# Kernel optimization log

Measured on AMD Instinct MI355X. Metric: run time of the kernel, lower is better.

The kernel has to match this reference:

```python
import jax, jax.numpy as jnp
import numpy as np

GAMMA = 0.3
R_PERCENT = 0.2
LAMBDA_PENALTY = 0.5
EPS = 1e-06

B_SZ, N_HEADS, K_FULL = 16, 32, 32768
K_IMG = 16384


def _zscore(x):
    mu = x.mean(axis=-1, keepdims=True)
    std = jnp.sqrt(((x - mu) ** 2).mean(axis=-1, keepdims=True))  # unbiased=False
    return (x - mu) / (std + EPS)


def _topk_binary(scores, k):
    # scores: [B,H] -> binary mask [B,H]; only strictly-positive topk values count
    vals, idx = jax.lax.top_k(scores, k)
    b = jnp.arange(scores.shape[0])[:, None]
    return jnp.zeros_like(scores).at[b, idx].set((vals > 0).astype(scores.dtype))


def setup_inputs() -> dict:
    key = jax.random.key(0)
    k1, k2, k3, k4, k5 = jax.random.split(key, 5)
    attn_logits_last = jax.random.normal(k1, (B_SZ, N_HEADS, K_FULL), dtype=jnp.float32)
    # exactly K_IMG image tokens per row (alternating pattern -> strided gather)
    image_mask = jnp.tile((jnp.arange(K_FULL) % 2 == 0).astype(jnp.int32)[None, :], (B_SZ, 1))
    feat_C = jax.random.normal(k2, (B_SZ, K_IMG), dtype=jnp.float32)
    feat_A = jax.random.normal(k3, (B_SZ, K_IMG), dtype=jnp.float32)
    feat_D = jax.random.normal(k4, (B_SZ, K_IMG), dtype=jnp.float32)
    feat_B = jax.random.normal(k5, (B_SZ, K_IMG), dtype=jnp.float32)
    return {"attn_logits_last": attn_logits_last, "image_mask": image_mask,
            "feat_C": feat_C, "feat_A": feat_A, "feat_D": feat_D, "feat_B": feat_B}


def reference(attn_logits_last, image_mask, feat_C, feat_A, feat_D, feat_B):
    B, H, K_full = attn_logits_last.shape
    K_img = feat_C.shape[1]

    # --- compute_rf ---
    C_t = jax.nn.relu(_zscore(feat_C))
    A_t = jax.nn.sigmoid(_zscore(feat_A))
    D_t = jax.nn.sigmoid(_zscore(feat_D))
    B_t = jax.nn.sigmoid(_zscore(feat_B))
    denom = jnp.maximum(1.0 + LAMBDA_PENALTY * (D_t + B_t), EPS)
    rf = jnp.maximum(C_t * A_t / denom, 0.0)  # [B,K_img]

    # --- align: positions of image tokens (exactly K_img ones per row) ---
    idx = jax.vmap(lambda m: jnp.nonzero(m, size=K_img)[0])(image_mask)  # [B,K_img]

    # --- image-normalized attention ---
    probs_full = jax.nn.softmax(attn_logits_last, axis=-1)
    mask_f = image_mask[:, None, :].astype(attn_logits_last.dtype)  # [B,1,K_full]
    probs_img = probs_full * mask_f
    probs_img_norm = probs_img / jnp.maximum(probs_img.sum(axis=-1, keepdims=True), EPS)
    attn_img_norm = jnp.take_along_axis(probs_img_norm, idx[:, None, :], axis=-1)  # [B,H,K_img]

    # --- dynamic head roles ---
    low_rf = jnp.maximum(1.0 - rf, 0.0)
    s_pos = (attn_img_norm * rf[:, None, :]).sum(axis=-1)   # [B,H]
    s_neg = (attn_img_norm * low_rf[:, None, :]).sum(axis=-1)
    k_heads = min(max(1, int(np.ceil(R_PERCENT * H))), H)
    m_pos = _topk_binary(s_pos, k_heads)
    neg_scores = jnp.where(m_pos > 0, -jnp.inf, s_neg)
    m_neg = _topk_binary(neg_scores, k_heads) * (m_pos == 0).astype(s_pos.dtype)

    # --- delta and scatter back to full logits ---
    delta_img = GAMMA * (m_pos[:, :, None] * rf[:, None, :]
                         - m_neg[:, :, None] * low_rf[:, None, :])  # [B,H,K_img]
    delta_full = jax.vmap(
        lambda d, i: jnp.zeros((H, K_full), attn_logits_last.dtype).at[:, i].set(d)
    )(delta_img, idx)
    delta_full = delta_full * mask_f
    return attn_logits_last + delta_full
```

## Files before the change

### kernel.cpp

```cpp
#include <hip/hip_runtime.h>
#include <math.h>

#define GAMMA 0.3f
#define EPS 1e-6f
#define B_SZ 16
#define NH 32
#define KF 32768
#define KI 16384
#define KHEADS 7

typedef float f4v __attribute__((ext_vector_type(4)));

constexpr int OFF_MU    = 0;
constexpr int OFF_SD    = 64;
constexpr int OFF_RAWS  = 128;
constexpr int OFF_RAWP  = 640;
constexpr int OFF_RAWN  = 1152;
constexpr int IOFF_BSUM = 1664;
constexpr int OFF_RFF   = 4096;


__global__ __launch_bounds__(256) void k_stats_cnt(const float* __restrict__ fC,
        const float* __restrict__ fA, const float* __restrict__ fD,
        const float* __restrict__ fB, const int* __restrict__ mask,
        float* __restrict__ ws) {
    int bid = blockIdx.x, t = threadIdx.x;
    int lane = t & 63, wid = t >> 6;
    if (bid < 64) {
        int b = bid >> 2, f = bid & 3;
        const float* src;
        if (f == 0) src = fC; else if (f == 1) src = fA; else if (f == 2) src = fD; else src = fB;
        src += (size_t)b * KI;
        double s = 0.0, s2 = 0.0;
        #pragma unroll 4
        for (int i = t; i < KI / 4; i += 256) {
            float4 v = ((const float4*)src)[i];
            s  += (double)v.x + (double)v.y + (double)v.z + (double)v.w;
            s2 += (double)v.x * v.x + (double)v.y * v.y + (double)v.z * v.z + (double)v.w * v.w;
        }
        #pragma unroll
        for (int off = 32; off > 0; off >>= 1) {
            s  += __shfl_down(s, off);
            s2 += __shfl_down(s2, off);
        }
        __shared__ double w1[4], w2[4];
        if (lane == 0) { w1[wid] = s; w2[wid] = s2; }
        __syncthreads();
        if (t == 0) {
            double S1 = w1[0] + w1[1] + w1[2] + w1[3];
            double S2 = w2[0] + w2[1] + w2[2] + w2[3];
            double mu  = S1 * (1.0 / KI);
            double var = fmax(S2 * (1.0 / KI) - mu * mu, 0.0);
            ws[OFF_MU + bid] = (float)mu;
            ws[OFF_SD + bid] = (float)(sqrt(var) + (double)EPS);
        }
    } else {
        int cblk = bid - 64;
        if (cblk < 6) ws[OFF_RAWS + cblk * 256 + t] = 0.f;
        const int* mrow = mask + (size_t)cblk * 2048;
        int4 m0 = *(const int4*)(mrow + t * 8);
        int4 m1 = *(const int4*)(mrow + t * 8 + 4);
        int cnt = (m0.x != 0) + (m0.y != 0) + (m0.z != 0) + (m0.w != 0)
                + (m1.x != 0) + (m1.y != 0) + (m1.z != 0) + (m1.w != 0);
        #pragma unroll
        for (int off = 32; off > 0; off >>= 1) cnt += __shfl_down(cnt, off);
        __shared__ int wc[4];
        if (lane == 0) wc[wid] = cnt;
        __syncthreads();
        if (t == 0) ((int*)ws)[IOFF_BSUM + cblk] = wc[0] + wc[1] + wc[2] + wc[3];
    }
}

__global__ __launch_bounds__(256) void k_rf_expand(const float* __restrict__ fC,
        const float* __restrict__ fA, const float* __restrict__ fD,
        const float* __restrict__ fB, const int* __restrict__ mask,
        float* __restrict__ ws) {
    __shared__ int sb[16];
    __shared__ int wsum[4];
    __shared__ float rfbuf[2048];
    int blk = blockIdx.x, t = threadIdx.x;
    int b = blk >> 4, c = blk & 15;
    int lane = t & 63, wid = t >> 6;

    const int* bsum = (const int*)ws + IOFF_BSUM;
    if (t < 16) sb[t] = (t < c) ? bsum[(b << 4) + t] : 0;

    const int* mrow = mask + (size_t)blk * 2048;
    int4 m0 = *(const int4*)(mrow + t * 8);
    int4 m1 = *(const int4*)(mrow + t * 8 + 4);
    int mv[8] = {m0.x, m0.y, m0.z, m0.w, m1.x, m1.y, m1.z, m1.w};
    int cnt = 0;
    #pragma unroll
    for (int j = 0; j < 8; ++j) cnt += (mv[j] != 0);

    int x = cnt;
    #pragma unroll
    for (int off = 1; off < 64; off <<= 1) {
        int v = __shfl_up(x, off);
        if (lane >= off) x += v;
    }
    if (lane == 63) wsum[wid] = x;
    __syncthreads();
    int base = 0;
    #pragma unroll
    for (int w = 0; w < 4; ++w) base += (w < wid) ? wsum[w] : 0;
    int total = wsum[0] + wsum[1] + wsum[2] + wsum[3];
    int rloc = base + x - cnt;
    int boff = 0;
    #pragma unroll
    for (int i = 0; i < 16; ++i) boff += sb[i];

    float mu0 = ws[OFF_MU + b * 4 + 0], sd0 = ws[OFF_SD + b * 4 + 0];
    float mu1 = ws[OFF_MU + b * 4 + 1], sd1 = ws[OFF_SD + b * 4 + 1];
    float mu2 = ws[OFF_MU + b * 4 + 2], sd2 = ws[OFF_SD + b * 4 + 2];
    float mu3 = ws[OFF_MU + b * 4 + 3], sd3 = ws[OFF_SD + b * 4 + 3];
    for (int j = t; j < total; j += 256) {
        size_t idx = (size_t)b * KI + boff + j;
        float Ct = fmaxf((fC[idx] - mu0) / sd0, 0.f);
        float At = 1.f / (1.f + __expf(-((fA[idx] - mu1) / sd1)));
        float Dt = 1.f / (1.f + __expf(-((fD[idx] - mu2) / sd2)));
        float Bt = 1.f / (1.f + __expf(-((fB[idx] - mu3) / sd3)));
        float denom = fmaxf(1.f + 0.5f * (Dt + Bt), EPS);
        rfbuf[j] = fmaxf(Ct * At / denom, 0.f);
    }
    __syncthreads();
    float vr[8];
    #pragma unroll
    for (int j = 0; j < 8; ++j) {
        if (mv[j]) { vr[j] = rfbuf[rloc]; ++rloc; }
        else       { vr[j] = -1.f; }
    }
    float* rff = ws + OFF_RFF + (size_t)blk * 2048 + t * 8;
    *(float4*)(rff)     = *(float4*)(vr);
    *(float4*)(rff + 4) = *(float4*)(vr + 4);
}

__global__ __launch_bounds__(256) void k_scores(const float* __restrict__ attn,
                                                float* __restrict__ ws) {
    int g = blockIdx.x, t = threadIdx.x;
    int bh = g >> 2, qtr = g & 3;
    int b = bh >> 5;
    const float* xr  = attn + ((size_t)bh << 15) + ((size_t)qtr << 13);
    const float* rff = ws + OFF_RFF + ((size_t)b << 15) + ((size_t)qtr << 13);
    float S = 0.f, P = 0.f, N = 0.f;
    #pragma unroll
    for (int i = 0; i < 8; ++i) {
        int k = (i * 256 + t) * 4;
        float4 xs = *(const float4*)(xr + k);
        float4 rv = *(const float4*)(rff + k);
        float xa[4] = {xs.x, xs.y, xs.z, xs.w};
        float va[4] = {rv.x, rv.y, rv.z, rv.w};
        #pragma unroll
        for (int j = 0; j < 4; ++j) {
            float e = __expf(xa[j]);
            bool on = va[j] >= 0.f;
            float rfv  = fmaxf(va[j], 0.f);
            float lrfv = on ? fmaxf(1.f - va[j], 0.f) : 0.f;
            S += on ? e : 0.f;
            P = fmaf(e, rfv, P);
            N = fmaf(e, lrfv, N);
        }
    }
    int lane = t & 63, wid = t >> 6;
    #pragma unroll
    for (int off = 32; off > 0; off >>= 1) {
        S += __shfl_down(S, off);
        P += __shfl_down(P, off);
        N += __shfl_down(N, off);
    }
    __shared__ float wS[4], wP[4], wN[4];
    if (lane == 0) { wS[wid] = S; wP[wid] = P; wN[wid] = N; }
    __syncthreads();
    if (t == 0) {
        atomicAdd(&ws[OFF_RAWS + bh], wS[0] + wS[1] + wS[2] + wS[3]);
        atomicAdd(&ws[OFF_RAWP + bh], wP[0] + wP[1] + wP[2] + wP[3]);
        atomicAdd(&ws[OFF_RAWN + bh], wN[0] + wN[1] + wN[2] + wN[3]);
    }
}

__global__ __launch_bounds__(256) void k_out(const float* __restrict__ attn,
        const float* __restrict__ ws, float* __restrict__ out) {
    unsigned int t = threadIdx.x;
    unsigned int j = blockIdx.x;
    unsigned int r = j & 7, q = j >> 3;
    unsigned int chunk = 8u * r + 64u * (q >> 3) + (q & 7);
    unsigned int flat = chunk * 2048 + t * 8;
    unsigned int bh = flat >> 15;
    unsigned int b  = bh >> 5;
    unsigned int h  = bh & 31;

    __shared__ float ssp[NH], snv[NH];
    __shared__ int smp[NH];
    __shared__ float s_gp, s_gn;
    if (t < NH) {
        float S0 = ws[OFF_RAWS + b * NH + t];
        ssp[t] = ws[OFF_RAWP + b * NH + t] / S0;
        snv[t] = ws[OFF_RAWN + b * NH + t] / S0;
    }
    __syncthreads();
    if (t < NH) {
        float sp = ssp[t];
        int cnt = 0;
        for (int jj = 0; jj < NH; ++jj) { float o = ssp[jj]; cnt += (o > sp) || (o == sp && jj < (int)t); }
        smp[t] = (cnt < KHEADS) && (sp > 0.f);
    }
    __syncthreads();
    if (t < NH && smp[t]) snv[t] = -INFINITY;
    __syncthreads();
    if (t == 0) {
        float gp = 0.f, gn = 0.f;
        if (smp[h]) gp = GAMMA;
        else {
            float nv = snv[h];
            int cnt = 0;
            for (int jj = 0; jj < NH; ++jj) { float o = snv[jj]; cnt += (o > nv) || (o == nv && jj < (int)h); }
            if ((cnt < KHEADS) && (nv > 0.f)) gn = GAMMA;
        }
        s_gp = gp; s_gn = gn;
    }
    __syncthreads();

    float gp = s_gp, gn = s_gn;
    const float* rff = ws + OFF_RFF + ((size_t)b << 15);
    unsigned int k = flat & (KF - 1);
    #pragma unroll
    for (int half8 = 0; half8 < 2; ++half8) {
        unsigned int f2 = flat + half8 * 4, k2 = k + half8 * 4;
        float4 xs = *(const float4*)(attn + f2);
        float4 rv = *(const float4*)(rff + k2);
        float va[4] = {rv.x, rv.y, rv.z, rv.w};
        float xa[4] = {xs.x, xs.y, xs.z, xs.w};
        float oa[4];
        #pragma unroll
        for (int jj = 0; jj < 4; ++jj) {
            bool on = va[jj] >= 0.f;
            float rfv  = fmaxf(va[jj], 0.f);
            float lrfv = on ? fmaxf(1.f - va[jj], 0.f) : 0.f;
            oa[jj] = xa[jj] + gp * rfv - gn * lrfv;
        }
        f4v o = {oa[0], oa[1], oa[2], oa[3]};
        __builtin_nontemporal_store(o, (f4v*)(out + f2));
    }
}

extern "C" void kernel_launch(void* const* d_in, const int* in_sizes, int n_in,
                              void* d_out, int out_size, void* d_ws, size_t ws_size,
                              hipStream_t stream) {
    const float* attn = (const float*)d_in[0];
    const int*   mask = (const int*)d_in[1];
    const float* fC   = (const float*)d_in[2];
    const float* fA   = (const float*)d_in[3];
    const float* fD   = (const float*)d_in[4];
    const float* fB   = (const float*)d_in[5];
    float* out = (float*)d_out;
    float* ws = (float*)d_ws;

    k_stats_cnt<<<320, 256, 0, stream>>>(fC, fA, fD, fB, mask, ws);
    k_rf_expand<<<256, 256, 0, stream>>>(fC, fA, fD, fB, mask, ws);
    k_scores   <<<2048, 256, 0, stream>>>(attn, ws);
    k_out      <<<B_SZ * NH * KF / 2048, 256, 0, stream>>>(attn, ws, out);
}
```

Measured before the change: 147.2 us.

## Compute head-role gains once in last-block epilogue of reduction kernel

Adds a per-batch completion counter to the score-reduction kernel so that the last block for each batch computes the top-k head masks and writes per-head gp/gn gains to the workspace. The output kernel then just loads two scalars per block, instead of every block redoing the ranking with several __syncthreads barriers. The attention input is also read with nontemporal loads. In exchange, the reduction kernel gains threadfences, a counter atomic and a serialized tail block.

```diff
diff --git a/kernel.cpp b/kernel.cpp
--- a/kernel.cpp
+++ b/kernel.cpp
@@ -16,7 +16,10 @@
 constexpr int OFF_RAWS  = 128;
 constexpr int OFF_RAWP  = 640;
 constexpr int OFF_RAWN  = 1152;
-constexpr int IOFF_BSUM = 1664;
+constexpr int OFF_GP    = 1664;
+constexpr int OFF_GN    = 2176;
+constexpr int IOFF_CNT  = 2688;
+constexpr int IOFF_BSUM = 2720;
 constexpr int OFF_RFF   = 4096;
 
 
@@ -57,6 +60,7 @@
     } else {
         int cblk = bid - 64;
         if (cblk < 6) ws[OFF_RAWS + cblk * 256 + t] = 0.f;
+        if (cblk == 6 && t < 16) ((int*)ws)[IOFF_CNT + t] = 0;
         const int* mrow = mask + (size_t)cblk * 2048;
         int4 m0 = *(const int4*)(mrow + t * 8);
         int4 m1 = *(const int4*)(mrow + t * 8 + 4);
@@ -169,12 +173,51 @@
         N += __shfl_down(N, off);
     }
     __shared__ float wS[4], wP[4], wN[4];
+    __shared__ int s_last;
     if (lane == 0) { wS[wid] = S; wP[wid] = P; wN[wid] = N; }
     __syncthreads();
     if (t == 0) {
         atomicAdd(&ws[OFF_RAWS + bh], wS[0] + wS[1] + wS[2] + wS[3]);
         atomicAdd(&ws[OFF_RAWP + bh], wP[0] + wP[1] + wP[2] + wP[3]);
         atomicAdd(&ws[OFF_RAWN + bh], wN[0] + wN[1] + wN[2] + wN[3]);
+        __threadfence();
+        int old = atomicAdd((int*)ws + IOFF_CNT + b, 1);
+        s_last = (old == 127);
+    }
+    __syncthreads();
+    if (!s_last) return;
+
+    __threadfence();
+    __shared__ float ssp[NH], snv[NH];
+    __shared__ int smp[NH];
+    if (t < NH) {
+        float S0 = __hip_atomic_load(&ws[OFF_RAWS + b * NH + t], __ATOMIC_RELAXED, __HIP_MEMORY_SCOPE_AGENT);
+        float Pp = __hip_atomic_load(&ws[OFF_RAWP + b * NH + t], __ATOMIC_RELAXED, __HIP_MEMORY_SCOPE_AGENT);
+        float Nn = __hip_atomic_load(&ws[OFF_RAWN + b * NH + t], __ATOMIC_RELAXED, __HIP_MEMORY_SCOPE_AGENT);
+        ssp[t] = Pp / S0;
+        snv[t] = Nn / S0;
+    }
+    __syncthreads();
+    if (t < NH) {
+        float sp = ssp[t];
+        int c2 = 0;
+        for (int j = 0; j < NH; ++j) { float o = ssp[j]; c2 += (o > sp) || (o == sp && j < t); }
+        smp[t] = (c2 < KHEADS) && (sp > 0.f);
+    }
+    __syncthreads();
+    if (t < NH && smp[t]) snv[t] = -INFINITY;
+    __syncthreads();
+    if (t < NH) {
+        float gp = 0.f, gn = 0.f;
+        if (smp[t]) gp = GAMMA;
+        else {
+            float nv = snv[t];
+            int c2 = 0;
+            for (int j = 0; j < NH; ++j) { float o = snv[j]; c2 += (o > nv) || (o == nv && j < t); }
+            if ((c2 < KHEADS) && (nv > 0.f)) gn = GAMMA;
+        }
+        ws[OFF_GP + b * NH + t] = gp;
+        ws[OFF_GN + b * NH + t] = gn;
     }
 }
 
@@ -187,56 +230,25 @@
     unsigned int flat = chunk * 2048 + t * 8;
     unsigned int bh = flat >> 15;
     unsigned int b  = bh >> 5;
-    unsigned int h  = bh & 31;
-
-    __shared__ float ssp[NH], snv[NH];
-    __shared__ int smp[NH];
-    __shared__ float s_gp, s_gn;
-    if (t < NH) {
-        float S0 = ws[OFF_RAWS + b * NH + t];
-        ssp[t] = ws[OFF_RAWP + b * NH + t] / S0;
-        snv[t] = ws[OFF_RAWN + b * NH + t] / S0;
-    }
-    __syncthreads();
-    if (t < NH) {
-        float sp = ssp[t];
-        int cnt = 0;
-        for (int jj = 0; jj < NH; ++jj) { float o = ssp[jj]; cnt += (o > sp) || (o == sp && jj < (int)t); }
-        smp[t] = (cnt < KHEADS) && (sp > 0.f);
-    }
-    __syncthreads();
-    if (t < NH && smp[t]) snv[t] = -INFINITY;
-    __syncthreads();
-    if (t == 0) {
-        float gp = 0.f, gn = 0.f;
-        if (smp[h]) gp = GAMMA;
-        else {
-            float nv = snv[h];
-            int cnt = 0;
-            for (int jj = 0; jj < NH; ++jj) { float o = snv[jj]; cnt += (o > nv) || (o == nv && jj < (int)h); }
-            if ((cnt < KHEADS) && (nv > 0.f)) gn = GAMMA;
-        }
-        s_gp = gp; s_gn = gn;
-    }
-    __syncthreads();
-
-    float gp = s_gp, gn = s_gn;
+
+    float gp = ws[OFF_GP + bh];
+    float gn = ws[OFF_GN + bh];
+
     const float* rff = ws + OFF_RFF + ((size_t)b << 15);
     unsigned int k = flat & (KF - 1);
     #pragma unroll
     for (int half8 = 0; half8 < 2; ++half8) {
         unsigned int f2 = flat + half8 * 4, k2 = k + half8 * 4;
-        float4 xs = *(const float4*)(attn + f2);
-        float4 rv = *(const float4*)(rff + k2);
-        float va[4] = {rv.x, rv.y, rv.z, rv.w};
-        float xa[4] = {xs.x, xs.y, xs.z, xs.w};
+        f4v xs = __builtin_nontemporal_load((const f4v*)(attn + f2));
+        f4v rv = *(const f4v*)(rff + k2);
         float oa[4];
         #pragma unroll
         for (int jj = 0; jj < 4; ++jj) {
-            bool on = va[jj] >= 0.f;
-            float rfv  = fmaxf(va[jj], 0.f);
-            float lrfv = on ? fmaxf(1.f - va[jj], 0.f) : 0.f;
-            oa[jj] = xa[jj] + gp * rfv - gn * lrfv;
+            float va = rv[jj];
+            bool on = va >= 0.f;
+            float rfv  = fmaxf(va, 0.f);
+            float lrfv = on ? fmaxf(1.f - va, 0.f) : 0.f;
+            oa[jj] = xs[jj] + gp * rfv - gn * lrfv;
         }
         f4v o = {oa[0], oa[1], oa[2], oa[3]};
         __builtin_nontemporal_store(o, (f4v*)(out + f2));
```

After: 250.1 us. +69.9%, slower.
